# Performance work log

Measured on AMD Instinct MI355X. Metric: run time of the kernel, lower is better.

## Reference

```python
import jax, jax.numpy as jnp
import numpy as np

V = 100000   # vocab_size / n_nodes
D = 128      # embedding_dim
B = 16384    # batch of items
S = 64       # samples per item
E = 640000   # edges


def setup_inputs() -> dict:
    key = jax.random.key(0)
    k1, k2, k3, k4, k5 = jax.random.split(key, 5)
    items = jax.random.randint(k1, (B,), 0, V)
    samples = jax.random.randint(k2, (B, S), 0, V)
    edge_index = jax.random.randint(k3, (2, E), 0, V)
    # xavier_uniform for embedding table and GCN linear weight
    emb_lim = float(np.sqrt(6.0 / (V + D)))
    emb_weight = jax.random.uniform(k4, (V, D), minval=-emb_lim, maxval=emb_lim, dtype=jnp.float32)
    w_lim = float(np.sqrt(6.0 / (D + D)))
    gcn_weight = jax.random.uniform(k5, (D, D), minval=-w_lim, maxval=w_lim, dtype=jnp.float32)
    gcn_bias = jnp.zeros((D,), dtype=jnp.float32)
    return {"items": items, "samples": samples, "edge_index": edge_index,
            "emb_weight": emb_weight, "gcn_weight": gcn_weight, "gcn_bias": gcn_bias}


def gcn_conv(x, edge_index, W, b, num_nodes):
    """PyG GCNConv: add self-loops, symmetric D^-1/2 (A+I) D^-1/2 normalization,
    linear transform, scatter-add aggregation, bias."""
    h = x @ W  # [N, D]
    loops = jnp.arange(num_nodes)
    src = jnp.concatenate([edge_index[0], loops])  # source nodes j
    dst = jnp.concatenate([edge_index[1], loops])  # target nodes i
    deg = jax.ops.segment_sum(jnp.ones_like(src, dtype=h.dtype), dst, num_segments=num_nodes)
    deg_inv_sqrt = jnp.where(deg > 0, jax.lax.rsqrt(jnp.maximum(deg, 1.0)), 0.0)
    norm = deg_inv_sqrt[src] * deg_inv_sqrt[dst]  # [E+N]
    msgs = norm[:, None] * h[src]                  # gather-scale
    out = jax.ops.segment_sum(msgs, dst, num_segments=num_nodes)  # scatter-add
    return out + b


def reference(items, samples, edge_index, emb_weight, gcn_weight, gcn_bias):
    nodes = gcn_conv(emb_weight, edge_index, gcn_weight, gcn_bias, emb_weight.shape[0])  # [V, D]
    item_emb = nodes[items]      # [B, D]
    sample_emb = nodes[samples]  # [B, S, D]
    # bmm([B,1,D], [B,D,S]).squeeze(1) == einsum
    scores = jnp.einsum('bd,bsd->bs', item_emb, sample_emb)
    return scores
```

## Files before the change

kernel.cpp:

```cpp
#include <hip/hip_runtime.h>
#include <hip/hip_bf16.h>

#define V_NODES 100000
#define DIM 128
#define BATCH 16384
#define SAMP 64
#define NEDGE 640000
#define NSAMP (BATCH * SAMP)

__device__ __forceinline__ float bl(unsigned u) { return __uint_as_float(u << 16); }
__device__ __forceinline__ float bh(unsigned u) { return __uint_as_float(u & 0xffff0000u); }
__device__ __forceinline__ unsigned short f2bf(float x) {
    unsigned u = __float_as_uint(x);
    return (unsigned short)((u + 0x7fffu + ((u >> 16) & 1u)) >> 16);
}

typedef __attribute__((ext_vector_type(8))) short bf16x8;
typedef __attribute__((ext_vector_type(4))) float f32x4;

__global__ void k_zero(int4* __restrict__ p, int n4) {
    int i = blockIdx.x * blockDim.x + threadIdx.x;
    if (i < n4) p[i] = make_int4(0, 0, 0, 0);
}

__global__ void k_wcvt(const float* __restrict__ W, unsigned short* __restrict__ wt_bf) {
    int g = blockIdx.x * blockDim.x + threadIdx.x;
    int n = g & 127;
    int k4 = (g >> 7) << 2;
    ushort4 o;
    o.x = f2bf(W[(k4 + 0) * 128 + n]);
    o.y = f2bf(W[(k4 + 1) * 128 + n]);
    o.z = f2bf(W[(k4 + 2) * 128 + n]);
    o.w = f2bf(W[(k4 + 3) * 128 + n]);
    *(ushort4*)(wt_bf + n * 128 + k4) = o;
}

__global__ void k_count(const int* __restrict__ key, int* __restrict__ cnt, int E) {
    int e = blockIdx.x * blockDim.x + threadIdx.x;
    if (e < E) atomicAdd(&cnt[key[e]], 1);
}

__global__ void k_bsum(const int* __restrict__ cnt, int* __restrict__ bsum, int V) {
    __shared__ int red[4];
    int b = blockIdx.x, t = threadIdx.x;
    int s = 0;
    int base = b * 1024;
    for (int i = 0; i < 4; ++i) {
        int idx = base + i * 256 + t;
        if (idx < V) s += cnt[idx];
    }
    for (int m = 32; m >= 1; m >>= 1) s += __shfl_xor(s, m, 64);
    int lane = t & 63, wid = t >> 6;
    if (lane == 0) red[wid] = s;
    __syncthreads();
    if (t == 0) bsum[b] = red[0] + red[1] + red[2] + red[3];
}

__global__ void k_bscan(const int* __restrict__ bsum, int* __restrict__ boff, int nb) {
    int l = threadIdx.x;
    int i0 = 2 * l, i1 = 2 * l + 1;
    int v0 = (i0 < nb) ? bsum[i0] : 0;
    int v1 = (i1 < nb) ? bsum[i1] : 0;
    int s = v0 + v1;
    int x = s;
    for (int off = 1; off < 64; off <<= 1) {
        int n = __shfl_up(x, off, 64);
        if (l >= off) x += n;
    }
    int excl = x - s;
    if (i0 < nb) boff[i0] = excl;
    if (i1 < nb) boff[i1] = excl + v0;
}

__global__ void k_offs(const int* __restrict__ cnt, const int* __restrict__ boff,
                       int* __restrict__ offs, float* __restrict__ dinv,
                       int* __restrict__ cursor, int V) {
    __shared__ int wsum[4];
    int b = blockIdx.x, t = threadIdx.x;
    int lane = t & 63, wid = t >> 6;
    int base = b * 1024 + t * 4;
    int c[4];
    for (int j = 0; j < 4; ++j) {
        int idx = base + j;
        c[j] = (idx < V) ? cnt[idx] : 0;
    }
    int tot = c[0] + c[1] + c[2] + c[3];
    int x = tot;
    for (int off = 1; off < 64; off <<= 1) {
        int n = __shfl_up(x, off, 64);
        if (lane >= off) x += n;
    }
    int lex = x - tot;
    if (lane == 63) wsum[wid] = x;
    __syncthreads();
    int wpre = 0;
    for (int w = 0; w < wid; ++w) wpre += wsum[w];
    int o = boff[b] + wpre + lex;
    int pre = 0;
    for (int j = 0; j < 4; ++j) {
        int idx = base + j;
        if (idx < V) {
            int o0 = o + pre;
            offs[idx] = o0;
            cursor[idx] = o0;
            dinv[idx] = 1.0f / sqrtf((float)(c[j] + 1));
        }
        pre += c[j];
    }
}

__global__ void k_fill(const int* __restrict__ src, const int* __restrict__ dst,
                       int* __restrict__ cursor, int* __restrict__ csr, int E) {
    int e = blockIdx.x * blockDim.x + threadIdx.x;
    if (e < E) {
        int pos = atomicAdd(&cursor[dst[e]], 1);
        csr[pos] = src[e];
    }
}

__global__ __launch_bounds__(256) void k_hgemm(const float* __restrict__ emb,
                      unsigned short* __restrict__ h_bf,
                      const unsigned short* __restrict__ wt_bf, int V) {
    __shared__ unsigned short WtL[128 * 128];
    int t = threadIdx.x;
    int rowbase = blockIdx.x * 64;
    for (int i = 0; i < 8; ++i) {
        int j = t + i * 256;
        int n = j >> 4, c8 = (j & 15) << 3;
        uint4 v = *(const uint4*)(wt_bf + n * 128 + c8);
        *(uint4*)&WtL[n * 128 + (c8 ^ ((n & 7) << 3))] = v;
    }
    int wid = t >> 6, lane = t & 63;
    int r16  = lane & 15;
    int kgrp = lane >> 4;
    int grow = rowbase + wid * 16 + r16;
    const float* arow = emb + (size_t)grow * 128 + kgrp * 8;
    bool ok = (grow < V);
    float4 af[8];
    #pragma unroll
    for (int ks = 0; ks < 4; ++ks) {
        af[2 * ks]     = ok ? *(const float4*)(arow + ks * 32)     : make_float4(0.f, 0.f, 0.f, 0.f);
        af[2 * ks + 1] = ok ? *(const float4*)(arow + ks * 32 + 4) : make_float4(0.f, 0.f, 0.f, 0.f);
    }
    __syncthreads();
    f32x4 acc[8] = {};
    #pragma unroll
    for (int ks = 0; ks < 4; ++ks) {
        float4 a0 = af[2 * ks], a1 = af[2 * ks + 1];
        bf16x8 a;
        a[0] = (short)f2bf(a0.x); a[1] = (short)f2bf(a0.y);
        a[2] = (short)f2bf(a0.z); a[3] = (short)f2bf(a0.w);
        a[4] = (short)f2bf(a1.x); a[5] = (short)f2bf(a1.y);
        a[6] = (short)f2bf(a1.z); a[7] = (short)f2bf(a1.w);
        int kc = ks * 32 + kgrp * 8;
        #pragma unroll
        for (int n = 0; n < 8; ++n) {
            int wr = n * 16 + r16;
            bf16x8 b = *(const bf16x8*)&WtL[wr * 128 + (kc ^ ((wr & 7) << 3))];
            acc[n] = __builtin_amdgcn_mfma_f32_16x16x32_bf16(a, b, acc[n], 0, 0, 0);
        }
    }
    __syncthreads();
    #pragma unroll
    for (int n = 0; n < 8; ++n) {
        #pragma unroll
        for (int r = 0; r < 4; ++r) {
            int drow = wid * 16 + kgrp * 4 + r;
            int dcol = n * 16 + r16;
            WtL[drow * 128 + (dcol ^ ((drow & 7) << 3))] = f2bf(acc[n][r]);
        }
    }
    __syncthreads();
    for (int i = 0; i < 4; ++i) {
        int j = t + i * 256;
        int r = j >> 4, c8 = (j & 15) << 3;
        uint4 v = *(const uint4*)&WtL[r * 128 + (c8 ^ ((r & 7) << 3))];
        int gr = rowbase + r;
        if (gr < V) *(uint4*)(h_bf + (size_t)gr * 128 + c8) = v;
    }
}

__global__ __launch_bounds__(256) void k_agg(const unsigned short* __restrict__ h_bf,
                     const int* __restrict__ offs, const int* __restrict__ cnt,
                     const int* __restrict__ csr, const float* __restrict__ dinv,
                     const float* __restrict__ bias,
                     unsigned* __restrict__ nodes_h, int V) {
    int wid = threadIdx.x >> 6;
    int lane = threadIdx.x & 63;
    int v = blockIdx.x * 4 + wid;
    if (v >= V) return;
    float dv = dinv[v];
    int beg = offs[v], num = cnt[v];
    int nid = 0; float nw = 0.0f;
    if (lane < num) {
        nid = csr[beg + lane];
        nw = dinv[nid];
    }
    unsigned u0 = ((const unsigned*)(h_bf + (size_t)v * DIM))[lane];
    float wself = dv * dv;
    float2 bv = ((const float2*)bias)[lane];
    float ax = bv.x + wself * bl(u0), ay = bv.y + wself * bh(u0);
    float cx = 0.f, cy = 0.f;
    int n0 = min(num, 64);
    int i = 0;
    for (; i + 4 <= n0; i += 4) {
        int s0 = __shfl(nid, i,     64);
        int s1 = __shfl(nid, i + 1, 64);
        int s2 = __shfl(nid, i + 2, 64);
        int s3 = __shfl(nid, i + 3, 64);
        float w0 = dv * __shfl(nw, i,     64);
        float w1 = dv * __shfl(nw, i + 1, 64);
        float w2 = dv * __shfl(nw, i + 2, 64);
        float w3 = dv * __shfl(nw, i + 3, 64);
        unsigned e0 = ((const unsigned*)(h_bf + (size_t)s0 * DIM))[lane];
        unsigned e1 = ((const unsigned*)(h_bf + (size_t)s1 * DIM))[lane];
        unsigned e2 = ((const unsigned*)(h_bf + (size_t)s2 * DIM))[lane];
        unsigned e3 = ((const unsigned*)(h_bf + (size_t)s3 * DIM))[lane];
        ax += w0 * bl(e0); ay += w0 * bh(e0);
        cx += w1 * bl(e1); cy += w1 * bh(e1);
        ax += w2 * bl(e2); ay += w2 * bh(e2);
        cx += w3 * bl(e3); cy += w3 * bh(e3);
    }
    for (; i < n0; ++i) {
        int s = __shfl(nid, i, 64);
        float w = dv * __shfl(nw, i, 64);
        unsigned u = ((const unsigned*)(h_bf + (size_t)s * DIM))[lane];
        ax += w * bl(u); ay += w * bh(u);
    }
    for (int k = 64; k < num; ++k) {
        int s = csr[beg + k];
        float w = dv * dinv[s];
        unsigned u = ((const unsigned*)(h_bf + (size_t)s * DIM))[lane];
        ax += w * bl(u); ay += w * bh(u);
    }
    ax += cx; ay += cy;
    nodes_h[(size_t)v * (DIM / 2) + lane] =
        (unsigned)f2bf(ax) | ((unsigned)f2bf(ay) << 16);
}

__global__ __launch_bounds__(256) void k_score(const unsigned short* __restrict__ nodes_h,
                      const int* __restrict__ items, const int* __restrict__ samples,
                      float* __restrict__ out) {
    int b = blockIdx.x;
    int t = threadIdx.x;
    int q = t & 3;
    int sidx = t >> 2;
    int item = items[b];
    const uint4* irow = (const uint4*)(nodes_h + (size_t)item * DIM) + q * 4;
    uint4 a[4];
    #pragma unroll
    for (int c = 0; c < 4; ++c) a[c] = irow[c];

    int j = samples[b * SAMP + sidx];
    const uint4* srow = (const uint4*)(nodes_h + (size_t)j * DIM) + q * 4;
    uint4 s4[4];
    #pragma unroll
    for (int c = 0; c < 4; ++c) s4[c] = srow[c];

    float p = 0.f;
    #pragma unroll
    for (int c = 0; c < 4; ++c) {
        uint4 av = a[c], sv = s4[c];
        p += bl(av.x) * bl(sv.x) + bh(av.x) * bh(sv.x);
        p += bl(av.y) * bl(sv.y) + bh(av.y) * bh(sv.y);
        p += bl(av.z) * bl(sv.z) + bh(av.z) * bh(sv.z);
        p += bl(av.w) * bl(sv.w) + bh(av.w) * bh(sv.w);
    }
    p += __shfl_xor(p, 1, 64);
    p += __shfl_xor(p, 2, 64);
    if (q == 0) out[b * SAMP + sidx] = p;
}

extern "C" void kernel_launch(void* const* d_in, const int* in_sizes, int n_in,
                              void* d_out, int out_size, void* d_ws, size_t ws_size,
                              hipStream_t stream) {
    const int*   items   = (const int*)d_in[0];
    const int*   samples = (const int*)d_in[1];
    const int*   edges   = (const int*)d_in[2];
    const float* emb     = (const float*)d_in[3];
    const float* W       = (const float*)d_in[4];
    const float* bias    = (const float*)d_in[5];
    float* out = (float*)d_out;

    char* ws = (char*)d_ws;
    int*   cnt    = (int*)(ws + 0);
    int*   cursor = (int*)(ws + (512 << 10));
    float* dinv   = (float*)(ws + (1 << 20));
    int*   offs   = (int*)(ws + 3 * (512 << 10));
    int*   bsum   = (int*)(ws + (2 << 20));
    int*   boff   = (int*)(ws + (2 << 20) + (4 << 10));
    unsigned short* wt_bf = (unsigned short*)(ws + (3 << 20));
    int*   csr    = (int*)(ws + (4 << 20));
    unsigned short* h_bf    = (unsigned short*)(ws + (8 << 20));
    unsigned*       nodes_h = (unsigned*)(ws + (34 << 20));

    const int* esrc = edges;
    const int* edst = edges + NEDGE;

    int nb = (V_NODES + 1023) / 1024;
    k_zero <<<98, 256, 0, stream>>>((int4*)cnt, V_NODES / 4);
    k_wcvt <<<16, 256, 0, stream>>>(W, wt_bf);
    k_count<<<(NEDGE + 255) / 256, 256, 0, stream>>>(edst, cnt, NEDGE);
    k_bsum <<<nb, 256, 0, stream>>>(cnt, bsum, V_NODES);
    k_bscan<<<1, 64, 0, stream>>>(bsum, boff, nb);
    k_offs <<<nb, 256, 0, stream>>>(cnt, boff, offs, dinv, cursor, V_NODES);
    k_fill <<<(NEDGE + 255) / 256, 256, 0, stream>>>(esrc, edst, cursor, csr, NEDGE);
    k_hgemm<<<(V_NODES + 63) / 64, 256, 0, stream>>>(emb, h_bf, wt_bf, V_NODES);
    k_agg  <<<(V_NODES + 3) / 4, 256, 0, stream>>>(h_bf, offs, cnt, csr, dinv, bias, nodes_h, V_NODES);
    k_score<<<BATCH, 256, 0, stream>>>((const unsigned short*)nodes_h, items, samples, out);
}
```

Baseline: 172.4 us.

## Process two nodes per wave in aggregation; read GEMM weights from global

The aggregation kernel now assigns two destination nodes to each wavefront and interleaves their neighbor gathers, halving the grid and exposing more independent loads per wave to hide gather latency. Separately, the GEMM kernel stops staging the 32KB bf16 weight matrix into shared memory and reads B fragments directly from global (cache-resident), cutting LDS use and a barrier so more blocks can be resident. Risks: more registers in the aggregation kernel, imbalance between paired nodes' degrees, and uncoalesced repeated global weight reads in the GEMM.

```diff
diff --git a/kernel.cpp b/kernel.cpp
--- a/kernel.cpp
+++ b/kernel.cpp
@@ -121,15 +121,9 @@
 __global__ __launch_bounds__(256) void k_hgemm(const float* __restrict__ emb,
                       unsigned short* __restrict__ h_bf,
                       const unsigned short* __restrict__ wt_bf, int V) {
-    __shared__ unsigned short WtL[128 * 128];
+    __shared__ unsigned short DsL[64 * 128];
     int t = threadIdx.x;
     int rowbase = blockIdx.x * 64;
-    for (int i = 0; i < 8; ++i) {
-        int j = t + i * 256;
-        int n = j >> 4, c8 = (j & 15) << 3;
-        uint4 v = *(const uint4*)(wt_bf + n * 128 + c8);
-        *(uint4*)&WtL[n * 128 + (c8 ^ ((n & 7) << 3))] = v;
-    }
     int wid = t >> 6, lane = t & 63;
     int r16  = lane & 15;
     int kgrp = lane >> 4;
@@ -142,7 +136,6 @@
         af[2 * ks]     = ok ? *(const float4*)(arow + ks * 32)     : make_float4(0.f, 0.f, 0.f, 0.f);
         af[2 * ks + 1] = ok ? *(const float4*)(arow + ks * 32 + 4) : make_float4(0.f, 0.f, 0.f, 0.f);
     }
-    __syncthreads();
     f32x4 acc[8] = {};
     #pragma unroll
     for (int ks = 0; ks < 4; ++ks) {
@@ -155,26 +148,24 @@
         int kc = ks * 32 + kgrp * 8;
         #pragma unroll
         for (int n = 0; n < 8; ++n) {
-            int wr = n * 16 + r16;
-            bf16x8 b = *(const bf16x8*)&WtL[wr * 128 + (kc ^ ((wr & 7) << 3))];
+            bf16x8 b = *(const bf16x8*)(wt_bf + (n * 16 + r16) * 128 + kc);
             acc[n] = __builtin_amdgcn_mfma_f32_16x16x32_bf16(a, b, acc[n], 0, 0, 0);
         }
     }
-    __syncthreads();
     #pragma unroll
     for (int n = 0; n < 8; ++n) {
         #pragma unroll
         for (int r = 0; r < 4; ++r) {
             int drow = wid * 16 + kgrp * 4 + r;
             int dcol = n * 16 + r16;
-            WtL[drow * 128 + (dcol ^ ((drow & 7) << 3))] = f2bf(acc[n][r]);
+            DsL[drow * 128 + (dcol ^ ((drow & 7) << 3))] = f2bf(acc[n][r]);
         }
     }
     __syncthreads();
     for (int i = 0; i < 4; ++i) {
         int j = t + i * 256;
         int r = j >> 4, c8 = (j & 15) << 3;
-        uint4 v = *(const uint4*)&WtL[r * 128 + (c8 ^ ((r & 7) << 3))];
+        uint4 v = *(const uint4*)&DsL[r * 128 + (c8 ^ ((r & 7) << 3))];
         int gr = rowbase + r;
         if (gr < V) *(uint4*)(h_bf + (size_t)gr * 128 + c8) = v;
     }
@@ -185,57 +176,92 @@
                      const int* __restrict__ csr, const float* __restrict__ dinv,
                      const float* __restrict__ bias,
                      unsigned* __restrict__ nodes_h, int V) {
-    int wid = threadIdx.x >> 6;
+    int wv = threadIdx.x >> 6;
     int lane = threadIdx.x & 63;
-    int v = blockIdx.x * 4 + wid;
-    if (v >= V) return;
-    float dv = dinv[v];
-    int beg = offs[v], num = cnt[v];
-    int nid = 0; float nw = 0.0f;
-    if (lane < num) {
-        nid = csr[beg + lane];
-        nw = dinv[nid];
-    }
-    unsigned u0 = ((const unsigned*)(h_bf + (size_t)v * DIM))[lane];
-    float wself = dv * dv;
+    int vA = blockIdx.x * 8 + wv * 2;
+    int vB = vA + 1;
+    if (vA >= V) return;
+    bool hasB = (vB < V);
+    float dvA = dinv[vA];
+    float dvB = hasB ? dinv[vB] : 0.f;
+    int begA = offs[vA], numA = cnt[vA];
+    int begB = hasB ? offs[vB] : 0, numB = hasB ? cnt[vB] : 0;
+    int nidA = 0, nidB = 0; float nwA = 0.f, nwB = 0.f;
+    if (lane < numA) { nidA = csr[begA + lane]; nwA = dinv[nidA]; }
+    if (lane < numB) { nidB = csr[begB + lane]; nwB = dinv[nidB]; }
+    unsigned u0A = ((const unsigned*)(h_bf + (size_t)vA * DIM))[lane];
+    unsigned u0B = hasB ? ((const unsigned*)(h_bf + (size_t)vB * DIM))[lane] : 0u;
     float2 bv = ((const float2*)bias)[lane];
-    float ax = bv.x + wself * bl(u0), ay = bv.y + wself * bh(u0);
-    float cx = 0.f, cy = 0.f;
-    int n0 = min(num, 64);
+    float axA = bv.x + dvA * dvA * bl(u0A), ayA = bv.y + dvA * dvA * bh(u0A);
+    float axB = bv.x + dvB * dvB * bl(u0B), ayB = bv.y + dvB * dvB * bh(u0B);
+    float cxA = 0.f, cyA = 0.f, cxB = 0.f, cyB = 0.f;
+    int nA = min(numA, 64), nB = min(numB, 64);
+    int m = min(nA, nB);
     int i = 0;
-    for (; i + 4 <= n0; i += 4) {
-        int s0 = __shfl(nid, i,     64);
-        int s1 = __shfl(nid, i + 1, 64);
-        int s2 = __shfl(nid, i + 2, 64);
-        int s3 = __shfl(nid, i + 3, 64);
-        float w0 = dv * __shfl(nw, i,     64);
-        float w1 = dv * __shfl(nw, i + 1, 64);
-        float w2 = dv * __shfl(nw, i + 2, 64);
-        float w3 = dv * __shfl(nw, i + 3, 64);
+    for (; i + 2 <= m; i += 2) {
+        int sA0 = __shfl(nidA, i, 64),     sB0 = __shfl(nidB, i, 64);
+        int sA1 = __shfl(nidA, i + 1, 64), sB1 = __shfl(nidB, i + 1, 64);
+        float wA0 = dvA * __shfl(nwA, i, 64),     wB0 = dvB * __shfl(nwB, i, 64);
+        float wA1 = dvA * __shfl(nwA, i + 1, 64), wB1 = dvB * __shfl(nwB, i + 1, 64);
+        unsigned eA0 = ((const unsigned*)(h_bf + (size_t)sA0 * DIM))[lane];
+        unsigned eB0 = ((const unsigned*)(h_bf + (size_t)sB0 * DIM))[lane];
+        unsigned eA1 = ((const unsigned*)(h_bf + (size_t)sA1 * DIM))[lane];
+        unsigned eB1 = ((const unsigned*)(h_bf + (size_t)sB1 * DIM))[lane];
+        axA += wA0 * bl(eA0); ayA += wA0 * bh(eA0);
+        axB += wB0 * bl(eB0); ayB += wB0 * bh(eB0);
+        cxA += wA1 * bl(eA1); cyA += wA1 * bh(eA1);
+        cxB += wB1 * bl(eB1); cyB += wB1 * bh(eB1);
+    }
+    int ia = i;
+    for (; ia + 2 <= nA; ia += 2) {
+        int s0 = __shfl(nidA, ia, 64), s1 = __shfl(nidA, ia + 1, 64);
+        float w0 = dvA * __shfl(nwA, ia, 64), w1 = dvA * __shfl(nwA, ia + 1, 64);
         unsigned e0 = ((const unsigned*)(h_bf + (size_t)s0 * DIM))[lane];
         unsigned e1 = ((const unsigned*)(h_bf + (size_t)s1 * DIM))[lane];
-        unsigned e2 = ((const unsigned*)(h_bf + (size_t)s2 * DIM))[lane];
-        unsigned e3 = ((const unsigned*)(h_bf + (size_t)s3 * DIM))[lane];
-        ax += w0 * bl(e0); ay += w0 * bh(e0);
-        cx += w1 * bl(e1); cy += w1 * bh(e1);
-        ax += w2 * bl(e2); ay += w2 * bh(e2);
-        cx += w3 * bl(e3); cy += w3 * bh(e3);
-    }
-    for (; i < n0; ++i) {
-        int s = __shfl(nid, i, 64);
-        float w = dv * __shfl(nw, i, 64);
+        axA += w0 * bl(e0); ayA += w0 * bh(e0);
+        cxA += w1 * bl(e1); cyA += w1 * bh(e1);
+    }
+    for (; ia < nA; ++ia) {
+        int s = __shfl(nidA, ia, 64);
+        float w = dvA * __shfl(nwA, ia, 64);
         unsigned u = ((const unsigned*)(h_bf + (size_t)s * DIM))[lane];
-        ax += w * bl(u); ay += w * bh(u);
-    }
-    for (int k = 64; k < num; ++k) {
-        int s = csr[beg + k];
-        float w = dv * dinv[s];
+        axA += w * bl(u); ayA += w * bh(u);
+    }
+    int ib = i;
+    for (; ib + 2 <= nB; ib += 2) {
+        int s0 = __shfl(nidB, ib, 64), s1 = __shfl(nidB, ib + 1, 64);
+        float w0 = dvB * __shfl(nwB, ib, 64), w1 = dvB * __shfl(nwB, ib + 1, 64);
+        unsigned e0 = ((const unsigned*)(h_bf + (size_t)s0 * DIM))[lane];
+        unsigned e1 = ((const unsigned*)(h_bf + (size_t)s1 * DIM))[lane];
+        axB += w0 * bl(e0); ayB += w0 * bh(e0);
+        cxB += w1 * bl(e1); cyB += w1 * bh(e1);
+    }
+    for (; ib < nB; ++ib) {
+        int s = __shfl(nidB, ib, 64);
+        float w = dvB * __shfl(nwB, ib, 64);
         unsigned u = ((const unsigned*)(h_bf + (size_t)s * DIM))[lane];
-        ax += w * bl(u); ay += w * bh(u);
-    }
-    ax += cx; ay += cy;
-    nodes_h[(size_t)v * (DIM / 2) + lane] =
-        (unsigned)f2bf(ax) | ((unsigned)f2bf(ay) << 16);
+        axB += w * bl(u); ayB += w * bh(u);
+    }
+    for (int k = 64; k < numA; ++k) {
+        int s = csr[begA + k];
+        float w = dvA * dinv[s];
+        unsigned u = ((const unsigned*)(h_bf + (size_t)s * DIM))[lane];
+        axA += w * bl(u); ayA += w * bh(u);
+    }
+    for (int k = 64; k < numB; ++k) {
+        int s = csr[begB + k];
+        float w = dvB * dinv[s];
+        unsigned u = ((const unsigned*)(h_bf + (size_t)s * DIM))[lane];
+        axB += w * bl(u); ayB += w * bh(u);
+    }
+    axA += cxA; ayA += cyA;
+    nodes_h[(size_t)vA * (DIM / 2) + lane] =
+        (unsigned)f2bf(axA) | ((unsigned)f2bf(ayA) << 16);
+    if (hasB) {
+        axB += cxB; ayB += cyB;
+        nodes_h[(size_t)vB * (DIM / 2) + lane] =
+            (unsigned)f2bf(axB) | ((unsigned)f2bf(ayB) << 16);
+    }
 }
 
 __global__ __launch_bounds__(256) void k_score(const unsigned short* __restrict__ nodes_h,
@@ -306,6 +332,6 @@
     k_offs <<<nb, 256, 0, stream>>>(cnt, boff, offs, dinv, cursor, V_NODES);
     k_fill <<<(NEDGE + 255) / 256, 256, 0, stream>>>(esrc, edst, cursor, csr, NEDGE);
     k_hgemm<<<(V_NODES + 63) / 64, 256, 0, stream>>>(emb, h_bf, wt_bf, V_NODES);
-    k_agg  <<<(V_NODES + 3) / 4, 256, 0, stream>>>(h_bf, offs, cnt, csr, dinv, bias, nodes_h, V_NODES);
+    k_agg  <<<(V_NODES + 7) / 8, 256, 0, stream>>>(h_bf, offs, cnt, csr, dinv, bias, nodes_h, V_NODES);
     k_score<<<BATCH, 256, 0, stream>>>((const unsigned short*)nodes_h, items, samples, out);
 }
```

New measurement: 189.1 us. 9.7% more time.
